# Optimization experiments

Hardware: AMD Instinct MI355X
Metric: run time of the kernel (lower is better)

Reference implementation:

```python
import jax, jax.numpy as jnp
import numpy as np

D_MODEL = 256
D_STATE = 16
D_CONV = 4
EXPAND = 2
N_LAYERS = 4
D_INNER = D_MODEL * EXPAND
BATCH, H, W = 64, 30, 30
LN_EPS = 1e-5


def setup_inputs() -> dict:
    key = jax.random.key(0)
    ks = jax.random.split(key, 16)
    s = 0.02
    L, d, di, n = N_LAYERS, D_MODEL, D_INNER, D_STATE
    return {
        "grid": jax.random.randint(ks[0], (BATCH, H, W), 0, 10, dtype=jnp.int32),
        "color_embed": jax.random.normal(ks[1], (10, d), dtype=jnp.float32) * s,
        "pos_embed": jax.random.normal(ks[2], (1, 900, d), dtype=jnp.float32),
        "in_w": jax.random.normal(ks[3], (L, d, 2 * di), dtype=jnp.float32) * s,
        "in_b": jnp.zeros((L, 2 * di), jnp.float32),
        "conv_w": jax.random.normal(ks[4], (L, di, 1, D_CONV), dtype=jnp.float32) * s,
        "conv_b": jnp.zeros((L, di), jnp.float32),
        "xproj_w": jax.random.normal(ks[5], (L, di, 2 * n), dtype=jnp.float32) * s,
        "xproj_b": jnp.zeros((L, 2 * n), jnp.float32),
        "A_log": jax.random.normal(ks[6], (L, di, n), dtype=jnp.float32),
        "Dp": jnp.ones((L, di), jnp.float32),
        "out_w": jax.random.normal(ks[7], (L, di, d), dtype=jnp.float32) * s,
        "out_b": jnp.zeros((L, d), jnp.float32),
        "ln_g": jnp.ones((d,), jnp.float32),
        "ln_b": jnp.zeros((d,), jnp.float32),
        "cnt1_w": jax.random.normal(ks[8], (d, d // 2), dtype=jnp.float32) * s,
        "cnt1_b": jnp.zeros((d // 2,), jnp.float32),
        "cnt2_w": jax.random.normal(ks[9], (d // 2, 1), dtype=jnp.float32) * s,
        "cnt2_b": jnp.zeros((1,), jnp.float32),
        "col1_w": jax.random.normal(ks[10], (d, d // 2), dtype=jnp.float32) * s,
        "col1_b": jnp.zeros((d // 2,), jnp.float32),
        "col2_w": jax.random.normal(ks[11], (d // 2, 10), dtype=jnp.float32) * s,
        "col2_b": jnp.zeros((10,), jnp.float32),
    }


def _silu(v):
    return v * jax.nn.sigmoid(v)


def _layernorm(x, g, b):
    mu = jnp.mean(x, axis=-1, keepdims=True)
    var = jnp.mean((x - mu) ** 2, axis=-1, keepdims=True)
    return (x - mu) * jax.lax.rsqrt(var + LN_EPS) * g + b


def _selective_scan(x, xw, xb, A_log, Dv):
    # x: [B, S, d_inner]
    Bsz, S, di = x.shape
    ssm = x @ xw + xb                               # [B, S, 2*N]
    delta = jax.nn.softplus(ssm[..., :D_STATE])     # [B, S, N]
    Bm = ssm[..., D_STATE:]                         # [B, S, N]
    A = -jnp.exp(A_log)                             # [d_inner, N]

    def step(h, t):
        x_t, d_t, b_t = t                           # [B,di], [B,N], [B,N]
        h = h * jnp.exp(A[None] * d_t[:, None, :]) + x_t[:, :, None] * b_t[:, None, :]
        y = jnp.einsum('bdn,bn->bd', h, b_t) + Dv * x_t
        return h, y

    h0 = jnp.zeros((Bsz, di, D_STATE), x.dtype)
    _, ys = jax.lax.scan(step, h0, (x.swapaxes(0, 1), delta.swapaxes(0, 1), Bm.swapaxes(0, 1)))
    return ys.swapaxes(0, 1)                        # [B, S, d_inner]


def _block(x, in_w, in_b, conv_w, conv_b, xw, xb, A_log, Dv, ow, ob):
    xr = x @ in_w + in_b                            # [B, S, 2*d_inner]
    xs, res = xr[..., :D_INNER], xr[..., D_INNER:]
    # causal depthwise conv1d (torch pads both sides then slices [:S])
    xc = jax.lax.conv_general_dilated(
        xs.swapaxes(1, 2), conv_w, window_strides=(1,), padding=[(D_CONV - 1, 0)],
        feature_group_count=D_INNER, dimension_numbers=('NCH', 'OIH', 'NCH'))
    xc = xc + conv_b[None, :, None]
    xs = _silu(xc.swapaxes(1, 2))
    y = _selective_scan(xs, xw, xb, A_log, Dv)
    y = y * _silu(res)
    return y @ ow + ob


def reference(grid, color_embed, pos_embed, in_w, in_b, conv_w, conv_b,
              xproj_w, xproj_b, A_log, Dp, out_w, out_b, ln_g, ln_b,
              cnt1_w, cnt1_b, cnt2_w, cnt2_b, col1_w, col1_b, col2_w, col2_b):
    B, h, w = grid.shape
    S = h * w
    x = color_embed[grid].reshape(B, S, D_MODEL) + pos_embed[:, :S, :]
    for l in range(N_LAYERS):
        x = x + _block(x, in_w[l], in_b[l], conv_w[l], conv_b[l],
                       xproj_w[l], xproj_b[l], A_log[l], Dp[l], out_w[l], out_b[l])
        x = _layernorm(x, ln_g, ln_b)
    final = x[:, -1, :]                             # [B, d_model]
    # dropout is identity in eval mode
    total_count = jax.nn.relu(jax.nn.relu(final @ cnt1_w + cnt1_b) @ cnt2_w + cnt2_b)
    color_counts = jax.nn.relu(jax.nn.relu(final @ col1_w + col1_b) @ col2_w + col2_b)
    return (total_count, color_counts)
```

## Files before the change

kernel.cpp:

```cpp
#include <hip/hip_runtime.h>
#include <cstdint>

#define D_MODELC 256
#define N_LAYERSC 4
#define BATCHC 64
#define SEQC 900
#define NCH 10
#define CT 90
#define SUB 45
#define LN_EPSF 1e-5f
#define LOG2E 1.44269504088896f

typedef __bf16 bf16x8 __attribute__((ext_vector_type(8)));
typedef __bf16 bf16x4 __attribute__((ext_vector_type(4)));
typedef float floatx4 __attribute__((ext_vector_type(4)));
typedef float floatx2 __attribute__((ext_vector_type(2)));

#if defined(__has_builtin)
#if __has_builtin(__builtin_amdgcn_exp2f)
#define EXP2F __builtin_amdgcn_exp2f
#endif
#endif
#ifndef EXP2F
#define EXP2F exp2f
#endif

__device__ inline float sp(float v) { return (v > 20.f) ? v : log1pf(__expf(v)); }
__device__ inline float silu(float v) { return v / (1.f + __expf(-v)); }

__global__ void wprep(const float* __restrict__ W, __bf16* __restrict__ Wb,
                      int K, int N, int kshift) {
  int l = blockIdx.y;
  int idx = blockIdx.x * 256 + threadIdx.x;
  if (idx >= N * K) return;
  int n = idx >> kshift, k = idx & (K - 1);
  Wb[(size_t)l * N * K + idx] = (__bf16)W[(size_t)l * K * N + (size_t)k * N + n];
}

__global__ void embed_kernel(const int* __restrict__ grid,
                             const float* __restrict__ cemb,
                             const float* __restrict__ pemb,
                             __bf16* __restrict__ xh, __bf16* __restrict__ xl) {
  int row = blockIdx.x;
  int c = threadIdx.x;
  int s = row % SEQC;
  int g = grid[row];
  float v = cemb[g * D_MODELC + c] + pemb[s * D_MODELC + c];
  size_t o = (size_t)row * D_MODELC + c;
  __bf16 hh = (__bf16)v;
  xh[o] = hh;
  xl[o] = (__bf16)(v - (float)hh);
}

#define GLDA 44
template<int MODE, bool GUARD>
__global__ __launch_bounds__(256) void gemm_bf16(
    const __bf16* __restrict__ A, const __bf16* __restrict__ W,
    const float* __restrict__ bias,
    __bf16* __restrict__ Cb, __bf16* __restrict__ Cg,
    int M, int N, int K, int nrow, int ncol) {
  __shared__ __attribute__((aligned(16))) __bf16 As[128 * GLDA];
  __shared__ __attribute__((aligned(16))) __bf16 Bs[128 * GLDA];
  int id = blockIdx.x;
  int row, col;
  {
    int fullsup = (nrow >> 3) * 8 * ncol;
    if (id < fullsup) {
      int per = ncol * 8;
      int s = id / per, r = id % per;
      col = r >> 3;
      row = (s << 3) + (r & 7);
    } else {
      int r = id - fullsup;
      int tr = nrow & 7;
      col = r / tr;
      row = (nrow & ~7) + r % tr;
    }
  }
  int tid = threadIdx.x, lane = tid & 63, w = tid >> 6;
  int bm = row * 128, bn = col * 128;
  int wm = (w >> 1) * 64, wn = (w & 1) * 64;
  int lm = lane & 15, kq = lane >> 4;
  bool wactive = !GUARD || (bn + wn < N);

  floatx4 acc[4][4];
  floatx4 zero = {0.f, 0.f, 0.f, 0.f};
  #pragma unroll
  for (int i = 0; i < 4; ++i)
    #pragma unroll
    for (int j = 0; j < 4; ++j) acc[i][j] = zero;

  int r0 = tid >> 1;
  int kb = (tid & 1) * 16;

  for (int k0 = 0; k0 < K; k0 += 32) {
    __syncthreads();
    {
      size_t aoff = (size_t)(bm + r0) * K + k0 + kb;
      *(bf16x8*)&As[r0 * GLDA + kb]     = *(const bf16x8*)&A[aoff];
      *(bf16x8*)&As[r0 * GLDA + kb + 8] = *(const bf16x8*)&A[aoff + 8];
      int nr = bn + r0;
      if (!GUARD || nr < N) {
        size_t boff = (size_t)nr * K + k0 + kb;
        *(bf16x8*)&Bs[r0 * GLDA + kb]     = *(const bf16x8*)&W[boff];
        *(bf16x8*)&Bs[r0 * GLDA + kb + 8] = *(const bf16x8*)&W[boff + 8];
      } else {
        uint4 zu = make_uint4(0, 0, 0, 0);
        *(uint4*)&Bs[r0 * GLDA + kb] = zu;
        *(uint4*)&Bs[r0 * GLDA + kb + 8] = zu;
      }
    }
    __syncthreads();
    if (wactive) {
      bf16x8 fa[4], fb[4];
      #pragma unroll
      for (int mt = 0; mt < 4; ++mt)
        fa[mt] = *(const bf16x8*)&As[(wm + mt * 16 + lm) * GLDA + kq * 8];
      #pragma unroll
      for (int nt = 0; nt < 4; ++nt)
        fb[nt] = *(const bf16x8*)&Bs[(wn + nt * 16 + lm) * GLDA + kq * 8];
      #pragma unroll
      for (int mt = 0; mt < 4; ++mt)
        #pragma unroll
        for (int nt = 0; nt < 4; ++nt)
          acc[mt][nt] = __builtin_amdgcn_mfma_f32_16x16x32_bf16(fa[mt], fb[nt], acc[mt][nt], 0, 0, 0);
    }
  }

  if (!wactive) return;
  #pragma unroll
  for (int mt = 0; mt < 4; ++mt)
    #pragma unroll
    for (int nt = 0; nt < 4; ++nt) {
      int col2 = bn + wn + nt * 16 + lm;
      if (GUARD && col2 >= N) continue;
      float bz = bias[col2];
      #pragma unroll
      for (int i = 0; i < 4; ++i) {
        int rr = bm + wm + mt * 16 + kq * 4 + i;
        float v = acc[mt][nt][i] + bz;
        if (MODE == 1) {
          if (col2 < 16) v = sp(v);
          Cb[(size_t)rr * N + col2] = (__bf16)v;
        } else if (MODE == 2) {
          if (col2 < 512) Cb[(size_t)rr * 512 + col2] = (__bf16)v;
          else            Cg[(size_t)rr * 512 + col2 - 512] = (__bf16)silu(v);
        } else {
          Cb[(size_t)rr * N + col2] = (__bf16)v;
        }
      }
    }
}

__global__ __launch_bounds__(256) void conv_silu(
    const __bf16* __restrict__ xs, const float* __restrict__ cw,
    const float* __restrict__ cb, __bf16* __restrict__ xc, int total) {
  int idx = blockIdx.x * 256 + threadIdx.x;
  if (idx >= total) return;
  int d8 = (idx & 63) * 8;
  int g4 = idx >> 6;
  int bt0 = g4 * 4;
  int t0 = bt0 % SEQC;
  const __bf16* base = xs + (size_t)(bt0 - t0) * 512 + d8;
  float wv[8][4];
  #pragma unroll
  for (int e = 0; e < 8; ++e) {
    float4 wq = *(const float4*)&cw[(d8 + e) * 4];
    wv[e][0] = wq.x; wv[e][1] = wq.y; wv[e][2] = wq.z; wv[e][3] = wq.w;
  }
  float4 b0 = *(const float4*)&cb[d8];
  float4 b1 = *(const float4*)&cb[d8 + 4];
  float bb[8] = {b0.x, b0.y, b0.z, b0.w, b1.x, b1.y, b1.z, b1.w};
  float xw[7][8];
  #pragma unroll
  for (int j = 0; j < 7; ++j) {
    int ts = t0 - 3 + j;
    if (ts >= 0) {
      bf16x8 v = *(const bf16x8*)&base[(size_t)ts * 512];
      #pragma unroll
      for (int e = 0; e < 8; ++e) xw[j][e] = (float)v[e];
    } else {
      #pragma unroll
      for (int e = 0; e < 8; ++e) xw[j][e] = 0.f;
    }
  }
  #pragma unroll
  for (int i = 0; i < 4; ++i) {
    bf16x8 o;
    #pragma unroll
    for (int e = 0; e < 8; ++e) {
      float acc = bb[e];
      #pragma unroll
      for (int j = 0; j < 4; ++j) acc = fmaf(wv[e][j], xw[i + j][e], acc);
      o[e] = (__bf16)silu(acc);
    }
    *(bf16x8*)&xc[(size_t)(bt0 + i) * 512 + d8] = o;
  }
}

__global__ __launch_bounds__(256, 4) void scan_phase1(
    const __bf16* __restrict__ ssm, const float* __restrict__ A_log,
    const __bf16* __restrict__ xc,
    __bf16* __restrict__ hend, __bf16* __restrict__ Pp) {
  __shared__ float sb[SUB * 32];
  __shared__ __bf16 xsb[SUB * 256];
  int b = blockIdx.x, half = blockIdx.y, c = blockIdx.z;
  int tid = threadIdx.x;
  int dg0 = half * 256;
  int d = dg0 + tid;
  floatx2 a2p[8];
  #pragma unroll
  for (int n = 0; n < 8; ++n) {
    a2p[n][0] = -__expf(A_log[d * 16 + 2 * n]) * LOG2E;
    a2p[n][1] = -__expf(A_log[d * 16 + 2 * n + 1]) * LOG2E;
  }
  floatx2 h2[8], S2[8];
  #pragma unroll
  for (int n = 0; n < 8; ++n) { h2[n] = floatx2{0.f, 0.f}; S2[n] = floatx2{0.f, 0.f}; }
  size_t rowbase = (size_t)b * SEQC + c * CT;

  for (int sub = 0; sub < 2; ++sub) {
    int ts0 = sub * SUB;
    __syncthreads();
    for (int i = tid; i < SUB * 8; i += 256) {
      int tt = i >> 3, n4 = (i & 7) * 4;
      bf16x4 v = *(const bf16x4*)&ssm[(rowbase + ts0 + tt) * 32 + n4];
      float4 f = {(float)v[0], (float)v[1], (float)v[2], (float)v[3]};
      *(float4*)&sb[tt * 32 + n4] = f;
    }
    for (int i = tid; i < SUB * 64; i += 256) {
      int tt = i >> 6, j4 = (i & 63) * 4;
      *(bf16x4*)&xsb[tt * 256 + j4] =
          *(const bf16x4*)&xc[(rowbase + ts0 + tt) * 512 + dg0 + j4];
    }
    __syncthreads();
    for (int tt = 0; tt < SUB; ++tt) {
      const floatx2* dv2 = (const floatx2*)&sb[tt * 32];
      floatx2 del2[8], Bv2[8];
      #pragma unroll
      for (int n = 0; n < 8; ++n) { del2[n] = dv2[n]; Bv2[n] = dv2[8 + n]; }
      float xv = (float)xsb[tt * 256 + tid];
      floatx2 xv2 = {xv, xv};
      #pragma unroll
      for (int n = 0; n < 8; ++n) {
        S2[n] += del2[n];
        floatx2 t2 = a2p[n] * del2[n];
        floatx2 e2;
        e2[0] = EXP2F(t2[0]); e2[1] = EXP2F(t2[1]);
        h2[n] = h2[n] * e2 + xv2 * Bv2[n];
      }
    }
  }
  size_t base = ((size_t)(b * NCH + c) * 512 + d) * 16;
  bf16x8 h0, h1, p0, p1;
  #pragma unroll
  for (int n = 0; n < 4; ++n) {
    h0[2 * n] = (__bf16)h2[n][0];     h0[2 * n + 1] = (__bf16)h2[n][1];
    h1[2 * n] = (__bf16)h2[n + 4][0]; h1[2 * n + 1] = (__bf16)h2[n + 4][1];
    p0[2 * n] = (__bf16)EXP2F(a2p[n][0] * S2[n][0]);
    p0[2 * n + 1] = (__bf16)EXP2F(a2p[n][1] * S2[n][1]);
    p1[2 * n] = (__bf16)EXP2F(a2p[n + 4][0] * S2[n + 4][0]);
    p1[2 * n + 1] = (__bf16)EXP2F(a2p[n + 4][1] * S2[n + 4][1]);
  }
  *(bf16x8*)&hend[base] = h0; *(bf16x8*)&hend[base + 8] = h1;
  *(bf16x8*)&Pp[base] = p0;   *(bf16x8*)&Pp[base + 8] = p1;
}

__global__ __launch_bounds__(64) void scan_combine(
    __bf16* __restrict__ hend, const __bf16* __restrict__ Pp) {
  int b = blockIdx.x;
  int d = blockIdx.y * 64 + threadIdx.x;
  float hp[16] = {};
  for (int c = 0; c < NCH; ++c) {
    size_t base = ((size_t)(b * NCH + c) * 512 + d) * 16;
    bf16x8 he0 = *(const bf16x8*)&hend[base];
    bf16x8 he1 = *(const bf16x8*)&hend[base + 8];
    bf16x8 pp0 = *(const bf16x8*)&Pp[base];
    bf16x8 pp1 = *(const bf16x8*)&Pp[base + 8];
    bf16x8 o0, o1;
    #pragma unroll
    for (int n = 0; n < 8; ++n) {
      o0[n] = (__bf16)hp[n]; o1[n] = (__bf16)hp[n + 8];
      hp[n]     = fmaf((float)pp0[n], hp[n],     (float)he0[n]);
      hp[n + 8] = fmaf((float)pp1[n], hp[n + 8], (float)he1[n]);
    }
    *(bf16x8*)&hend[base] = o0; *(bf16x8*)&hend[base + 8] = o1;
  }
}

__global__ __launch_bounds__(256, 4) void scan_phase3(
    const __bf16* __restrict__ ssm, const float* __restrict__ A_log,
    const float* __restrict__ Dp, const __bf16* __restrict__ xc,
    const __bf16* __restrict__ gate, const __bf16* __restrict__ hin,
    __bf16* __restrict__ yc) {
  __shared__ float sb[SUB * 32];
  __shared__ __bf16 xsb[SUB * 256];
  int b = blockIdx.x, half = blockIdx.y, c = blockIdx.z;
  int tid = threadIdx.x;
  int dg0 = half * 256;
  int d = dg0 + tid;
  floatx2 a2p[8];
  #pragma unroll
  for (int n = 0; n < 8; ++n) {
    a2p[n][0] = -__expf(A_log[d * 16 + 2 * n]) * LOG2E;
    a2p[n][1] = -__expf(A_log[d * 16 + 2 * n + 1]) * LOG2E;
  }
  float Dv = Dp[d];
  floatx2 h2[8];
  {
    size_t base = ((size_t)(b * NCH + c) * 512 + d) * 16;
    bf16x8 h0 = *(const bf16x8*)&hin[base];
    bf16x8 h1 = *(const bf16x8*)&hin[base + 8];
    #pragma unroll
    for (int n = 0; n < 4; ++n) {
      h2[n][0] = (float)h0[2 * n];     h2[n][1] = (float)h0[2 * n + 1];
      h2[n + 4][0] = (float)h1[2 * n]; h2[n + 4][1] = (float)h1[2 * n + 1];
    }
  }
  size_t rowbase = (size_t)b * SEQC + c * CT;

  for (int sub = 0; sub < 2; ++sub) {
    int ts0 = sub * SUB;
    __syncthreads();
    for (int i = tid; i < SUB * 8; i += 256) {
      int tt = i >> 3, n4 = (i & 7) * 4;
      bf16x4 v = *(const bf16x4*)&ssm[(rowbase + ts0 + tt) * 32 + n4];
      float4 f = {(float)v[0], (float)v[1], (float)v[2], (float)v[3]};
      *(float4*)&sb[tt * 32 + n4] = f;
    }
    for (int i = tid; i < SUB * 64; i += 256) {
      int tt = i >> 6, j4 = (i & 63) * 4;
      *(bf16x4*)&xsb[tt * 256 + j4] =
          *(const bf16x4*)&xc[(rowbase + ts0 + tt) * 512 + dg0 + j4];
    }
    __syncthreads();
    for (int tt = 0; tt < SUB; ++tt) {
      const floatx2* dv2 = (const floatx2*)&sb[tt * 32];
      floatx2 del2[8], Bv2[8];
      #pragma unroll
      for (int n = 0; n < 8; ++n) { del2[n] = dv2[n]; Bv2[n] = dv2[8 + n]; }
      float xv = (float)xsb[tt * 256 + tid];
      floatx2 xv2 = {xv, xv};
      floatx2 yq[4];
      #pragma unroll
      for (int q = 0; q < 4; ++q) yq[q] = floatx2{0.f, 0.f};
      #pragma unroll
      for (int n = 0; n < 8; ++n) {
        floatx2 t2 = a2p[n] * del2[n];
        floatx2 e2;
        e2[0] = EXP2F(t2[0]); e2[1] = EXP2F(t2[1]);
        h2[n] = h2[n] * e2 + xv2 * Bv2[n];
        yq[n & 3] = h2[n] * Bv2[n] + yq[n & 3];
      }
      float ysum = ((yq[0][0] + yq[0][1]) + (yq[1][0] + yq[1][1])) +
                   ((yq[2][0] + yq[2][1]) + (yq[3][0] + yq[3][1]));
      xsb[tt * 256 + tid] = (__bf16)fmaf(Dv, xv, ysum);
    }
    __syncthreads();
    for (int i = tid; i < SUB * 64; i += 256) {
      int tt = i >> 6, j4 = (i & 63) * 4;
      size_t o = (rowbase + ts0 + tt) * 512 + dg0 + j4;
      bf16x4 y4 = *(const bf16x4*)&xsb[tt * 256 + j4];
      bf16x4 g4 = *(const bf16x4*)&gate[o];
      bf16x4 r;
      #pragma unroll
      for (int e = 0; e < 4; ++e) r[e] = (__bf16)((float)y4[e] * (float)g4[e]);
      *(bf16x4*)&yc[o] = r;
    }
  }
}

__global__ __launch_bounds__(256) void add_ln(
    __bf16* __restrict__ xh, __bf16* __restrict__ xl,
    const __bf16* __restrict__ ob,
    const float* __restrict__ g, const float* __restrict__ bb) {
  int lane = threadIdx.x & 63;
  size_t base = ((size_t)blockIdx.x * 4 + (threadIdx.x >> 6)) * 256;
  bf16x4 h4 = *(const bf16x4*)&xh[base + lane * 4];
  bf16x4 l4 = *(const bf16x4*)&xl[base + lane * 4];
  bf16x4 o4 = *(const bf16x4*)&ob[base + lane * 4];
  float v[4];
  #pragma unroll
  for (int i = 0; i < 4; ++i) v[i] = (float)h4[i] + (float)l4[i] + (float)o4[i];
  float s = v[0] + v[1] + v[2] + v[3];
  #pragma unroll
  for (int off = 32; off > 0; off >>= 1) s += __shfl_down(s, off);
  float mu = __shfl(s, 0) * (1.f / 256.f);
  float var = 0.f;
  #pragma unroll
  for (int i = 0; i < 4; ++i) { float dd = v[i] - mu; var = fmaf(dd, dd, var); }
  #pragma unroll
  for (int off = 32; off > 0; off >>= 1) var += __shfl_down(var, off);
  float r = rsqrtf(__shfl(var, 0) * (1.f / 256.f) + LN_EPSF);
  float4 gv = *(const float4*)&g[lane * 4];
  float4 bv = *(const float4*)&bb[lane * 4];
  float gg[4] = {gv.x, gv.y, gv.z, gv.w};
  float bbv[4] = {bv.x, bv.y, bv.z, bv.w};
  bf16x4 hq, lq;
  #pragma unroll
  for (int i = 0; i < 4; ++i) {
    float o = (v[i] - mu) * r * gg[i] + bbv[i];
    __bf16 hh = (__bf16)o;
    hq[i] = hh;
    lq[i] = (__bf16)(o - (float)hh);
  }
  *(bf16x4*)&xh[base + lane * 4] = hq;
  *(bf16x4*)&xl[base + lane * 4] = lq;
}

__global__ void extract_final(const __bf16* __restrict__ xh,
                              const __bf16* __restrict__ xl,
                              float* __restrict__ fin) {
  int b = blockIdx.x;
  int c = threadIdx.x;
  size_t o = ((size_t)b * SEQC + (SEQC - 1)) * D_MODELC + c;
  fin[(size_t)b * 256 + c] = (float)xh[o] + (float)xl[o];
}

__global__ __launch_bounds__(128) void heads_kernel(
    const float* __restrict__ fin,
    const float* __restrict__ cnt1_w, const float* __restrict__ cnt1_b,
    const float* __restrict__ cnt2_w, const float* __restrict__ cnt2_b,
    const float* __restrict__ col1_w, const float* __restrict__ col1_b,
    const float* __restrict__ col2_w, const float* __restrict__ col2_b,
    float* __restrict__ out) {
  int b = blockIdx.x;
  int tid = threadIdx.x;
  __shared__ float f[256];
  __shared__ float hc[128];
  __shared__ float hl[128];
  f[tid] = fin[b * 256 + tid];
  f[tid + 128] = fin[b * 256 + tid + 128];
  __syncthreads();
  float s1 = cnt1_b[tid], s2 = col1_b[tid];
  for (int c = 0; c < 256; ++c) {
    float v = f[c];
    s1 = fmaf(v, cnt1_w[c * 128 + tid], s1);
    s2 = fmaf(v, col1_w[c * 128 + tid], s2);
  }
  hc[tid] = fmaxf(s1, 0.f);
  hl[tid] = fmaxf(s2, 0.f);
  __syncthreads();
  if (tid == 0) {
    float t = cnt2_b[0];
    for (int j = 0; j < 128; ++j) t = fmaf(hc[j], cnt2_w[j], t);
    out[b] = fmaxf(t, 0.f);
  }
  if (tid < 10) {
    float t = col2_b[tid];
    for (int j = 0; j < 128; ++j) t = fmaf(hl[j], col2_w[j * 10 + tid], t);
    out[64 + b * 10 + tid] = fmaxf(t, 0.f);
  }
}

extern "C" void kernel_launch(void* const* d_in, const int* in_sizes, int n_in,
                              void* d_out, int out_size, void* d_ws, size_t ws_size,
                              hipStream_t stream) {
  const int*   grid   = (const int*)d_in[0];
  const float* cemb   = (const float*)d_in[1];
  const float* pemb   = (const float*)d_in[2];
  const float* in_w   = (const float*)d_in[3];
  const float* in_b   = (const float*)d_in[4];
  const float* conv_w = (const float*)d_in[5];
  const float* conv_b = (const float*)d_in[6];
  const float* xproj_w= (const float*)d_in[7];
  const float* xproj_b= (const float*)d_in[8];
  const float* A_log  = (const float*)d_in[9];
  const float* Dp     = (const float*)d_in[10];
  const float* out_w  = (const float*)d_in[11];
  const float* out_b  = (const float*)d_in[12];
  const float* ln_g   = (const float*)d_in[13];
  const float* ln_b   = (const float*)d_in[14];
  const float* cnt1_w = (const float*)d_in[15];
  const float* cnt1_b = (const float*)d_in[16];
  const float* cnt2_w = (const float*)d_in[17];
  const float* cnt2_b = (const float*)d_in[18];
  const float* col1_w = (const float*)d_in[19];
  const float* col1_b = (const float*)d_in[20];
  const float* col2_w = (const float*)d_in[21];
  const float* col2_b = (const float*)d_in[22];

  const int R = BATCHC * SEQC;
  float* ws = (float*)d_ws;
  size_t off = 0;
  auto alloc = [&](size_t fl) { float* p = ws + off; off += (fl + 63) & ~(size_t)63; return p; };

  float*  fin   = alloc((size_t)BATCHC * 256);
  __bf16* wi    = (__bf16*)alloc((size_t)N_LAYERSC * 1024 * 256 / 2);
  __bf16* wx    = (__bf16*)alloc((size_t)N_LAYERSC * 32 * 512 / 2);
  __bf16* wo    = (__bf16*)alloc((size_t)N_LAYERSC * 256 * 512 / 2);
  __bf16* xh    = (__bf16*)alloc((size_t)R * 256 / 2);
  __bf16* xl    = (__bf16*)alloc((size_t)R * 256 / 2);
  __bf16* xsyc  = (__bf16*)alloc((size_t)R * 512 / 2);
  float*  gateob= alloc((size_t)R * 512 / 2);
  __bf16* xc    = (__bf16*)alloc((size_t)R * 512 / 2);
  __bf16* ssm   = (__bf16*)alloc((size_t)R * 32 / 2);
  __bf16* hend  = (__bf16*)alloc((size_t)BATCHC * NCH * 512 * 16 / 2);
  __bf16* Pp    = (__bf16*)alloc((size_t)BATCHC * NCH * 512 * 16 / 2);
  __bf16* gate  = (__bf16*)gateob;
  __bf16* obb   = (__bf16*)gateob;

  wprep<<<dim3(1024, N_LAYERSC), 256, 0, stream>>>(in_w, wi, 256, 1024, 8);
  wprep<<<dim3(64, N_LAYERSC), 256, 0, stream>>>(xproj_w, wx, 512, 32, 9);
  wprep<<<dim3(512, N_LAYERSC), 256, 0, stream>>>(out_w, wo, 512, 256, 9);

  embed_kernel<<<R, 256, 0, stream>>>(grid, cemb, pemb, xh, xl);

  const int NROW = R / 128;
  for (int l = 0; l < N_LAYERSC; ++l) {
    gemm_bf16<2, false><<<NROW * 8, 256, 0, stream>>>(
        xh, wi + (size_t)l * 1024 * 256, in_b + l * 1024,
        xsyc, gate, R, 1024, 256, NROW, 8);
    conv_silu<<<(R * 16 + 255) / 256, 256, 0, stream>>>(
        xsyc, conv_w + (size_t)l * 512 * 4, conv_b + l * 512, xc, R * 16);
    gemm_bf16<1, true><<<NROW, 256, 0, stream>>>(
        xc, wx + (size_t)l * 32 * 512, xproj_b + l * 32,
        ssm, nullptr, R, 32, 512, NROW, 1);
    scan_phase1<<<dim3(BATCHC, 2, NCH - 1), 256, 0, stream>>>(
        ssm, A_log + (size_t)l * 512 * 16, xc, hend, Pp);
    scan_combine<<<dim3(BATCHC, 8), 64, 0, stream>>>(hend, Pp);
    scan_phase3<<<dim3(BATCHC, 2, NCH), 256, 0, stream>>>(
        ssm, A_log + (size_t)l * 512 * 16, Dp + l * 512, xc, gate, hend, xsyc);
    gemm_bf16<3, false><<<NROW * 2, 256, 0, stream>>>(
        xsyc, wo + (size_t)l * 256 * 512, out_b + l * 256,
        obb, nullptr, R, 256, 512, NROW, 2);
    add_ln<<<R / 4, 256, 0, stream>>>(xh, xl, obb, ln_g, ln_b);
  }

  extract_final<<<BATCHC, 256, 0, stream>>>(xh, xl, fin);
  heads_kernel<<<BATCHC, 128, 0, stream>>>(
      fin, cnt1_w, cnt1_b, cnt2_w, cnt2_b, col1_w, col1_b, col2_w, col2_b,
      (float*)d_out);
}
```

Baseline: 1.602 ms.

## Drop LDS staging of x in scan kernels; load per-thread directly with software prefetch

Both scan kernels stop staging the xc tile (and, in phase 3, the y output) through shared memory. Each thread now reads its own xc element straight from global memory, and phase 3 multiplies by the gate and writes yc inside the time loop. The loop is double-buffered so the next timestep's operands are loaded while the current step computes, and the shared-memory footprint shrinks. In exchange, the global accesses become 2-byte per-thread loads and stores (coalesced across the wave but narrower), with load latency now sitting on the serial recurrence path.

```diff
diff --git a/kernel.cpp b/kernel.cpp
--- a/kernel.cpp
+++ b/kernel.cpp
@@ -203,7 +203,6 @@
     const __bf16* __restrict__ xc,
     __bf16* __restrict__ hend, __bf16* __restrict__ Pp) {
   __shared__ float sb[SUB * 32];
-  __shared__ __bf16 xsb[SUB * 256];
   int b = blockIdx.x, half = blockIdx.y, c = blockIdx.z;
   int tid = threadIdx.x;
   int dg0 = half * 256;
@@ -218,6 +217,26 @@
   #pragma unroll
   for (int n = 0; n < 8; ++n) { h2[n] = floatx2{0.f, 0.f}; S2[n] = floatx2{0.f, 0.f}; }
   size_t rowbase = (size_t)b * SEQC + c * CT;
+
+  floatx2 dA[8], BA[8], dB[8], BB[8];
+  float xA, xB;
+  auto loadt = [&](int ts0, int tt, floatx2* del, floatx2* Bv, float& xv) {
+    const floatx2* p = (const floatx2*)&sb[tt * 32];
+    #pragma unroll
+    for (int n = 0; n < 8; ++n) { del[n] = p[n]; Bv[n] = p[8 + n]; }
+    xv = (float)xc[(rowbase + ts0 + tt) * 512 + d];
+  };
+  auto stept = [&](floatx2* del, floatx2* Bv, float xv) {
+    floatx2 xv2 = {xv, xv};
+    #pragma unroll
+    for (int n = 0; n < 8; ++n) {
+      S2[n] += del[n];
+      floatx2 t2 = a2p[n] * del[n];
+      floatx2 e2;
+      e2[0] = EXP2F(t2[0]); e2[1] = EXP2F(t2[1]);
+      h2[n] = h2[n] * e2 + xv2 * Bv[n];
+    }
+  };
 
   for (int sub = 0; sub < 2; ++sub) {
     int ts0 = sub * SUB;
@@ -228,28 +247,15 @@
       float4 f = {(float)v[0], (float)v[1], (float)v[2], (float)v[3]};
       *(float4*)&sb[tt * 32 + n4] = f;
     }
-    for (int i = tid; i < SUB * 64; i += 256) {
-      int tt = i >> 6, j4 = (i & 63) * 4;
-      *(bf16x4*)&xsb[tt * 256 + j4] =
-          *(const bf16x4*)&xc[(rowbase + ts0 + tt) * 512 + dg0 + j4];
-    }
     __syncthreads();
-    for (int tt = 0; tt < SUB; ++tt) {
-      const floatx2* dv2 = (const floatx2*)&sb[tt * 32];
-      floatx2 del2[8], Bv2[8];
-      #pragma unroll
-      for (int n = 0; n < 8; ++n) { del2[n] = dv2[n]; Bv2[n] = dv2[8 + n]; }
-      float xv = (float)xsb[tt * 256 + tid];
-      floatx2 xv2 = {xv, xv};
-      #pragma unroll
-      for (int n = 0; n < 8; ++n) {
-        S2[n] += del2[n];
-        floatx2 t2 = a2p[n] * del2[n];
-        floatx2 e2;
-        e2[0] = EXP2F(t2[0]); e2[1] = EXP2F(t2[1]);
-        h2[n] = h2[n] * e2 + xv2 * Bv2[n];
-      }
-    }
+    loadt(ts0, 0, dA, BA, xA);
+    for (int tt = 0; tt < SUB - 1; tt += 2) {
+      loadt(ts0, tt + 1, dB, BB, xB);
+      stept(dA, BA, xA);
+      if (tt + 2 < SUB) loadt(ts0, tt + 2, dA, BA, xA);
+      stept(dB, BB, xB);
+    }
+    stept(dA, BA, xA);
   }
   size_t base = ((size_t)(b * NCH + c) * 512 + d) * 16;
   bf16x8 h0, h1, p0, p1;
@@ -294,7 +300,6 @@
     const __bf16* __restrict__ gate, const __bf16* __restrict__ hin,
     __bf16* __restrict__ yc) {
   __shared__ float sb[SUB * 32];
-  __shared__ __bf16 xsb[SUB * 256];
   int b = blockIdx.x, half = blockIdx.y, c = blockIdx.z;
   int tid = threadIdx.x;
   int dg0 = half * 256;
@@ -318,6 +323,36 @@
     }
   }
   size_t rowbase = (size_t)b * SEQC + c * CT;
+
+  floatx2 dA[8], BA[8], dB[8], BB[8];
+  float xA, xB;
+  auto loadt = [&](int ts0, int tt, floatx2* del, floatx2* Bv, float& xv) {
+    const floatx2* p = (const floatx2*)&sb[tt * 32];
+    #pragma unroll
+    for (int n = 0; n < 8; ++n) { del[n] = p[n]; Bv[n] = p[8 + n]; }
+    xv = (float)xc[(rowbase + ts0 + tt) * 512 + d];
+  };
+  auto stept = [&](int ts0, int tt, floatx2* del, floatx2* Bv, float xv) {
+    floatx2 xv2 = {xv, xv};
+    floatx2 yq0 = {0.f, 0.f}, yq1 = {0.f, 0.f}, yq2 = {0.f, 0.f}, yq3 = {0.f, 0.f};
+    #pragma unroll
+    for (int n = 0; n < 8; ++n) {
+      floatx2 t2 = a2p[n] * del[n];
+      floatx2 e2;
+      e2[0] = EXP2F(t2[0]); e2[1] = EXP2F(t2[1]);
+      h2[n] = h2[n] * e2 + xv2 * Bv[n];
+      if ((n & 3) == 0) yq0 = h2[n] * Bv[n] + yq0;
+      else if ((n & 3) == 1) yq1 = h2[n] * Bv[n] + yq1;
+      else if ((n & 3) == 2) yq2 = h2[n] * Bv[n] + yq2;
+      else yq3 = h2[n] * Bv[n] + yq3;
+    }
+    float ysum = ((yq0[0] + yq0[1]) + (yq1[0] + yq1[1])) +
+                 ((yq2[0] + yq2[1]) + (yq3[0] + yq3[1]));
+    float y = fmaf(Dv, xv, ysum);
+    size_t o = (rowbase + ts0 + tt) * 512 + d;
+    float g = (float)gate[o];
+    yc[o] = (__bf16)(y * g);
+  };
 
   for (int sub = 0; sub < 2; ++sub) {
     int ts0 = sub * SUB;
@@ -328,45 +363,15 @@
       float4 f = {(float)v[0], (float)v[1], (float)v[2], (float)v[3]};
       *(float4*)&sb[tt * 32 + n4] = f;
     }
-    for (int i = tid; i < SUB * 64; i += 256) {
-      int tt = i >> 6, j4 = (i & 63) * 4;
-      *(bf16x4*)&xsb[tt * 256 + j4] =
-          *(const bf16x4*)&xc[(rowbase + ts0 + tt) * 512 + dg0 + j4];
-    }
     __syncthreads();
-    for (int tt = 0; tt < SUB; ++tt) {
-      const floatx2* dv2 = (const floatx2*)&sb[tt * 32];
-      floatx2 del2[8], Bv2[8];
-      #pragma unroll
-      for (int n = 0; n < 8; ++n) { del2[n] = dv2[n]; Bv2[n] = dv2[8 + n]; }
-      float xv = (float)xsb[tt * 256 + tid];
-      floatx2 xv2 = {xv, xv};
-      floatx2 yq[4];
-      #pragma unroll
-      for (int q = 0; q < 4; ++q) yq[q] = floatx2{0.f, 0.f};
-      #pragma unroll
-      for (int n = 0; n < 8; ++n) {
-        floatx2 t2 = a2p[n] * del2[n];
-        floatx2 e2;
-        e2[0] = EXP2F(t2[0]); e2[1] = EXP2F(t2[1]);
-        h2[n] = h2[n] * e2 + xv2 * Bv2[n];
-        yq[n & 3] = h2[n] * Bv2[n] + yq[n & 3];
-      }
-      float ysum = ((yq[0][0] + yq[0][1]) + (yq[1][0] + yq[1][1])) +
-                   ((yq[2][0] + yq[2][1]) + (yq[3][0] + yq[3][1]));
-      xsb[tt * 256 + tid] = (__bf16)fmaf(Dv, xv, ysum);
-    }
-    __syncthreads();
-    for (int i = tid; i < SUB * 64; i += 256) {
-      int tt = i >> 6, j4 = (i & 63) * 4;
-      size_t o = (rowbase + ts0 + tt) * 512 + dg0 + j4;
-      bf16x4 y4 = *(const bf16x4*)&xsb[tt * 256 + j4];
-      bf16x4 g4 = *(const bf16x4*)&gate[o];
-      bf16x4 r;
-      #pragma unroll
-      for (int e = 0; e < 4; ++e) r[e] = (__bf16)((float)y4[e] * (float)g4[e]);
-      *(bf16x4*)&yc[o] = r;
-    }
+    loadt(ts0, 0, dA, BA, xA);
+    for (int tt = 0; tt < SUB - 1; tt += 2) {
+      loadt(ts0, tt + 1, dB, BB, xB);
+      stept(ts0, tt, dA, BA, xA);
+      if (tt + 2 < SUB) loadt(ts0, tt + 2, dA, BA, xA);
+      stept(ts0, tt + 1, dB, BB, xB);
+    }
+    stept(ts0, SUB - 1, dA, BA, xA);
   }
 }
 
```

After: 1.544 ms. 1.04x faster.
